# Kernel optimization log

Hardware: AMD Instinct MI355X
Metric: run time of the kernel (lower is better)

The kernel has to match this reference:

```python
import jax, jax.numpy as jnp
import numpy as np

NEG = -1e9  # finite stand-in for -inf so grads stay NaN-free
BLANK = 0

def _lse3(a, b, c):
    m = jnp.maximum(jnp.maximum(a, b), c)
    return m + jnp.log(jnp.exp(a - m) + jnp.exp(b - m) + jnp.exp(c - m))

def setup_inputs() -> dict:
    key = jax.random.key(0)
    k1, k2, k3, k4 = jax.random.split(key, 4)
    T, B, C, S = 1024, 128, 256, 128
    logits = jax.random.normal(k1, (T, B, C), dtype=jnp.float32)
    log_probs = jax.nn.log_softmax(logits, axis=-1)  # CTCLoss expects log-probs
    y = jax.random.randint(k2, (B, S), 1, C)                 # labels in [1, C), never blank
    input_lengths = jax.random.randint(k3, (B,), 768, T + 1)  # 768..T
    target_lengths = jax.random.randint(k4, (B,), 64, S + 1)  # 64..S
    return {"log_probs": log_probs, "y": y,
            "input_lengths": input_lengths, "target_lengths": target_lengths}

def _ctc_loss(log_probs, y, input_lengths, target_lengths):
    T, B, C = log_probs.shape
    S = y.shape[1]
    L = 2 * S + 1  # extended label sequence: blank, y1, blank, y2, ..., blank

    ext = jnp.zeros((B, L), dtype=y.dtype).at[:, 1::2].set(y)  # even slots = blank(0)
    pos = jnp.arange(L)
    prev2 = jnp.concatenate([jnp.full((B, 2), BLANK, dtype=ext.dtype), ext[:, :-2]], axis=1)
    allow_skip = (pos[None, :] >= 2) & (ext != BLANK) & (ext != prev2)  # [B, L]

    # init alpha at t=0: only s=0 (blank) and s=1 (first label) reachable
    lp0 = log_probs[0]  # [B, C]
    alpha0 = jnp.full((B, L), NEG, dtype=log_probs.dtype)
    alpha0 = alpha0.at[:, 0].set(lp0[:, BLANK])
    alpha0 = alpha0.at[:, 1].set(jnp.take_along_axis(lp0, ext[:, 1:2], axis=1)[:, 0])

    def step(alpha, xs):
        lp_t, t = xs  # lp_t: [B, C]
        a0 = alpha
        a1 = jnp.concatenate([jnp.full((B, 1), NEG, alpha.dtype), alpha[:, :-1]], axis=1)
        a2 = jnp.concatenate([jnp.full((B, 2), NEG, alpha.dtype), alpha[:, :-2]], axis=1)
        a2 = jnp.where(allow_skip, a2, NEG)
        emit = jnp.take_along_axis(lp_t, ext, axis=1)  # [B, L]
        new = _lse3(a0, a1, a2) + emit
        # freeze alpha for samples whose input has already ended
        new = jnp.where(t < input_lengths[:, None], new, alpha)
        return new, None

    ts = jnp.arange(1, T)
    alpha_T, _ = jax.lax.scan(step, alpha0, (log_probs[1:], ts))

    # final log-likelihood: logsumexp of alpha at positions 2*tl and 2*tl-1
    idx_hi = (2 * target_lengths)[:, None]       # [B,1]
    idx_lo = (2 * target_lengths - 1)[:, None]
    a_hi = jnp.take_along_axis(alpha_T, idx_hi, axis=1)[:, 0]
    a_lo = jnp.take_along_axis(alpha_T, idx_lo, axis=1)[:, 0]
    m = jnp.maximum(a_hi, a_lo)
    ll = m + jnp.log(jnp.exp(a_hi - m) + jnp.exp(a_lo - m))
    loss = -ll  # per-sample negative log-likelihood

    # zero_infinity=True: zero out infeasible (effectively -inf likelihood) samples
    loss = jnp.where(loss < 0.5 * (-NEG), loss, 0.0)

    # reduction='mean': divide each loss by its target length, then batch mean
    return jnp.mean(loss / target_lengths.astype(loss.dtype))

def reference(log_probs, y, input_lengths, target_lengths):
    return _ctc_loss(log_probs, y, input_lengths, target_lengths)
```

## Files before the change

kernel.cpp:

```cpp
#include <hip/hip_runtime.h>


#define PF 8
#define CTC_C 256

__device__ __forceinline__ void renorm(double& Oa, double& Ob, double& Ea,
                                       double& Eb, double& E128, double& logC) {
  double m = fmax(fmax(Oa, Ob), fmax(Ea, Eb));
#pragma unroll
  for (int off = 32; off > 0; off >>= 1)
    m = fmax(m, __shfl_xor(m, off));
  m = fmax(m, E128);
  if (m > 0.) {
    long long bits = __double_as_longlong(m);
    int eb = (int)((bits >> 52) & 0x7ff);
    int e = eb - 1022;
    double s = __longlong_as_double((long long)(2045 - eb) << 52);
    Oa *= s; Ob *= s; Ea *= s; Eb *= s; E128 *= s;
    logC += (double)e * 0.6931471805599453;
  }
}

__global__ __launch_bounds__(64)
void ctc_fwd(const float* __restrict__ lp, const int* __restrict__ y,
             const int* __restrict__ ilen, const int* __restrict__ tlen,
             float* __restrict__ out, int T, int B, int S) {
  const int b = blockIdx.x;
  const int l = threadIdx.x;
  const long rowstride = (long)B * CTC_C;

  const int len = ilen[b];
  const int tl  = tlen[b];

  const int ya = y[(size_t)b * S + 2 * l];
  const int yb = y[(size_t)b * S + 2 * l + 1];
  const int yprev = __shfl_up(yb, 1);
  const bool skipA = (l > 0) && (ya != yprev);
  const bool skipB = (yb != ya);

  const float* row0 = lp + (size_t)b * CTC_C;
  const int y0 = y[(size_t)b * S];
  double Ea = (l == 0) ? (double)__expf(row0[0])  : 0.;
  double Oa = (l == 0) ? (double)__expf(row0[y0]) : 0.;
  double Eb = 0., Ob = 0., E128 = 0.;
  double logC = 0.;

  float pA[PF], pB[PF], pQ[PF];
#pragma unroll
  for (int d = 0; d < PF; ++d) {
    int t = 1 + d; t = (t < T) ? t : (T - 1);
    const float* r = lp + (size_t)t * rowstride + (size_t)b * CTC_C;
    pA[d] = r[ya]; pB[d] = r[yb]; pQ[d] = r[0];
  }

  const int nsteps = len - 1;
  const int nchunks = nsteps / PF;
  int t0 = 1;

  for (int c = 0; c < nchunks; ++c) {
#pragma unroll
    for (int d = 0; d < PF; ++d) {
      const int t = t0 + d;
      double pa = (double)__expf(pA[d]);
      double pb = (double)__expf(pB[d]);
      double pq = (double)__expf(pQ[d]);
      int tn = t + PF; tn = (tn < T) ? tn : (T - 1);
      const float* r = lp + (size_t)tn * rowstride + (size_t)b * CTC_C;
      pA[d] = r[ya]; pB[d] = r[yb]; pQ[d] = r[0];

      double Opm1 = __shfl_up(Ob, 1);
      Opm1 = (l == 0) ? 0. : Opm1;
      double O127 = __shfl(Ob, 63);

      double nOa = (Oa + Ea + (skipA ? Opm1 : 0.)) * pa;
      double nOb = (Ob + Eb + (skipB ? Oa   : 0.)) * pb;
      double nEa = (Ea + Opm1) * pq;
      double nEb = (Eb + Oa) * pq;
      E128 = (E128 + O127) * pq;
      Oa = nOa; Ob = nOb; Ea = nEa; Eb = nEb;

      if ((d & 7) == 7) renorm(Oa, Ob, Ea, Eb, E128, logC);
    }
    t0 += PF;
  }

#pragma unroll
  for (int d = 0; d < PF; ++d) {
    const int t = t0 + d;
    if (t <= nsteps) {
      double pa = (double)__expf(pA[d]);
      double pb = (double)__expf(pB[d]);
      double pq = (double)__expf(pQ[d]);
      double Opm1 = __shfl_up(Ob, 1);
      Opm1 = (l == 0) ? 0. : Opm1;
      double O127 = __shfl(Ob, 63);
      double nOa = (Oa + Ea + (skipA ? Opm1 : 0.)) * pa;
      double nOb = (Ob + Eb + (skipB ? Oa   : 0.)) * pb;
      double nEa = (Ea + Opm1) * pq;
      double nEb = (Eb + Oa) * pq;
      E128 = (E128 + O127) * pq;
      Oa = nOa; Ob = nOb; Ea = nEa; Eb = nEb;
      if ((d & 7) == 7) renorm(Oa, Ob, Ea, Eb, E128, logC);
    }
  }

  double vEa = __shfl(Ea, (tl >> 1) & 63);
  double vEb = __shfl(Eb, (tl >> 1) & 63);
  double vhi = (tl == S) ? E128 : ((tl & 1) ? vEb : vEa);
  int s2 = tl - 1;
  double vOa = __shfl(Oa, (s2 >> 1) & 63);
  double vOb = __shfl(Ob, (s2 >> 1) & 63);
  double vlo = (s2 & 1) ? vOb : vOa;

  double sum = vhi + vlo;
  double loss;
  if (sum > 0.) {
    loss = -(logC + log(sum));
  } else {
    loss = 1e30;
  }
  if (!(loss < 5.0e8)) loss = 0.;
  float contrib = (float)(loss / (double)tl / (double)B);
  if (l == 0) atomicAdd(out, contrib);
}

extern "C" void kernel_launch(void* const* d_in, const int* in_sizes, int n_in,
                              void* d_out, int out_size, void* d_ws, size_t ws_size,
                              hipStream_t stream) {
  const float* lp   = (const float*)d_in[0];
  const int*   yy   = (const int*)d_in[1];
  const int*   ilen = (const int*)d_in[2];
  const int*   tlen = (const int*)d_in[3];
  float* out = (float*)d_out;

  int B = in_sizes[2];
  int S = in_sizes[1] / B;
  int T = in_sizes[0] / (B * CTC_C);

  hipMemsetAsync(out, 0, sizeof(float), stream);
  ctc_fwd<<<B, 64, 0, stream>>>(lp, yy, ilen, tlen, out, T, B, S);
}
```

Before: 297.3 us.

## Restructure CTC recurrence: biased exp2, branchless masks, single shuffle, sparser renorm

Replaces expf with exp2f on a fused multiply-add that adds a constant exponent bias (2^9) per step, and subtracts the bias analytically at the end. The per-step shuffle of Ob is reorganized so only one shuffle (of the new Ob) is needed and the per-lane E128 update no longer needs a broadcast. Skip conditions become multiplicative masks feeding fma, prefetch pointers are advanced incrementally, and renormalization runs every 16 steps instead of 8. This targets the serial per-timestep latency chain of the wave, at some risk of overflow or underflow margin since renorm is less frequent.

```diff
diff --git a/kernel.cpp b/kernel.cpp
--- a/kernel.cpp
+++ b/kernel.cpp
@@ -3,23 +3,9 @@
 
 #define PF 8
 #define CTC_C 256
-
-__device__ __forceinline__ void renorm(double& Oa, double& Ob, double& Ea,
-                                       double& Eb, double& E128, double& logC) {
-  double m = fmax(fmax(Oa, Ob), fmax(Ea, Eb));
-#pragma unroll
-  for (int off = 32; off > 0; off >>= 1)
-    m = fmax(m, __shfl_xor(m, off));
-  m = fmax(m, E128);
-  if (m > 0.) {
-    long long bits = __double_as_longlong(m);
-    int eb = (int)((bits >> 52) & 0x7ff);
-    int e = eb - 1022;
-    double s = __longlong_as_double((long long)(2045 - eb) << 52);
-    Oa *= s; Ob *= s; Ea *= s; Eb *= s; E128 *= s;
-    logC += (double)e * 0.6931471805599453;
-  }
-}
+#define EXP_BIAS 9.0f
+#define LOG2E 1.4426950408889634f
+#define LN2 0.6931471805599453
 
 __global__ __launch_bounds__(64)
 void ctc_fwd(const float* __restrict__ lp, const int* __restrict__ y,
@@ -27,7 +13,7 @@
              float* __restrict__ out, int T, int B, int S) {
   const int b = blockIdx.x;
   const int l = threadIdx.x;
-  const long rowstride = (long)B * CTC_C;
+  const size_t rowstride = (size_t)B * CTC_C;
 
   const int len = ilen[b];
   const int tl  = tlen[b];
@@ -35,51 +21,71 @@
   const int ya = y[(size_t)b * S + 2 * l];
   const int yb = y[(size_t)b * S + 2 * l + 1];
   const int yprev = __shfl_up(yb, 1);
-  const bool skipA = (l > 0) && (ya != yprev);
-  const bool skipB = (yb != ya);
+  const double maskA = (ya != yprev) ? 1.0 : 0.0;
+  const double maskB = (yb != ya) ? 1.0 : 0.0;
 
   const float* row0 = lp + (size_t)b * CTC_C;
   const int y0 = y[(size_t)b * S];
-  double Ea = (l == 0) ? (double)__expf(row0[0])  : 0.;
-  double Oa = (l == 0) ? (double)__expf(row0[y0]) : 0.;
-  double Eb = 0., Ob = 0., E128 = 0.;
-  double logC = 0.;
+  double Ea = (l == 0) ? (double)__expf(row0[0])  : 0.0;
+  double Oa = (l == 0) ? (double)__expf(row0[y0]) : 0.0;
+  double Eb = 0.0, Ob = 0.0, E128 = 0.0;
+  double Opm1 = 0.0;
+  int e_sum = 0;
 
   float pA[PF], pB[PF], pQ[PF];
+  {
+    const float* r = lp + rowstride + (size_t)b * CTC_C;
+    const float* rl = lp + (size_t)(T - 1) * rowstride + (size_t)b * CTC_C;
 #pragma unroll
-  for (int d = 0; d < PF; ++d) {
-    int t = 1 + d; t = (t < T) ? t : (T - 1);
-    const float* r = lp + (size_t)t * rowstride + (size_t)b * CTC_C;
-    pA[d] = r[ya]; pB[d] = r[yb]; pQ[d] = r[0];
+    for (int d = 0; d < PF; ++d) {
+      const float* rp = (1 + d <= T - 1) ? r : rl;
+      pA[d] = rp[ya]; pB[d] = rp[yb]; pQ[d] = rp[0];
+      r += rowstride;
+    }
   }
 
   const int nsteps = len - 1;
   const int nchunks = nsteps / PF;
+  const float* rlast = lp + (size_t)(T - 1) * rowstride + (size_t)b * CTC_C;
+  const float* rfill = lp + (size_t)(1 + PF) * rowstride + (size_t)b * CTC_C;
   int t0 = 1;
 
   for (int c = 0; c < nchunks; ++c) {
 #pragma unroll
     for (int d = 0; d < PF; ++d) {
       const int t = t0 + d;
-      double pa = (double)__expf(pA[d]);
-      double pb = (double)__expf(pB[d]);
-      double pq = (double)__expf(pQ[d]);
-      int tn = t + PF; tn = (tn < T) ? tn : (T - 1);
-      const float* r = lp + (size_t)tn * rowstride + (size_t)b * CTC_C;
-      pA[d] = r[ya]; pB[d] = r[yb]; pQ[d] = r[0];
+      const float* rp = (t + PF <= T - 1) ? rfill : rlast;
+      float nA = rp[ya], nB = rp[yb], nQ = rp[0];
+      rfill += rowstride;
 
-      double Opm1 = __shfl_up(Ob, 1);
-      Opm1 = (l == 0) ? 0. : Opm1;
-      double O127 = __shfl(Ob, 63);
+      float fa = exp2f(fmaf(pA[d], LOG2E, EXP_BIAS));
+      float fb = exp2f(fmaf(pB[d], LOG2E, EXP_BIAS));
+      float fq = exp2f(fmaf(pQ[d], LOG2E, EXP_BIAS));
+      pA[d] = nA; pB[d] = nB; pQ[d] = nQ;
+      double pa = (double)fa, pb = (double)fb, pq = (double)fq;
 
-      double nOa = (Oa + Ea + (skipA ? Opm1 : 0.)) * pa;
-      double nOb = (Ob + Eb + (skipB ? Oa   : 0.)) * pb;
+      double nOb = fma(maskB, Oa, Ob + Eb) * pb;
+      double up = __shfl_up(nOb, 1);
+      double nOa = fma(maskA, Opm1, Oa + Ea) * pa;
       double nEa = (Ea + Opm1) * pq;
       double nEb = (Eb + Oa) * pq;
-      E128 = (E128 + O127) * pq;
+      E128 = (E128 + Ob) * pq;
       Oa = nOa; Ob = nOb; Ea = nEa; Eb = nEb;
+      Opm1 = (l == 0) ? 0.0 : up;
 
-      if ((d & 7) == 7) renorm(Oa, Ob, Ea, Eb, E128, logC);
+      if (d == PF - 1 && (c & 1)) {
+        double m = fmax(fmax(Oa, Ob), fmax(Ea, Eb));
+        m = fmax(m, E128);
+#pragma unroll
+        for (int off = 32; off > 0; off >>= 1)
+          m = fmax(m, __shfl_xor(m, off));
+        long long bits = __double_as_longlong(m);
+        int eb2 = (int)((bits >> 52) & 0x7ff);
+        int e = eb2 - 1022;
+        double s = __longlong_as_double((long long)(2045 - eb2) << 52);
+        Oa *= s; Ob *= s; Ea *= s; Eb *= s; E128 *= s; Opm1 *= s;
+        e_sum += e;
+      }
     }
     t0 += PF;
   }
@@ -88,38 +94,39 @@
   for (int d = 0; d < PF; ++d) {
     const int t = t0 + d;
     if (t <= nsteps) {
-      double pa = (double)__expf(pA[d]);
-      double pb = (double)__expf(pB[d]);
-      double pq = (double)__expf(pQ[d]);
-      double Opm1 = __shfl_up(Ob, 1);
-      Opm1 = (l == 0) ? 0. : Opm1;
-      double O127 = __shfl(Ob, 63);
-      double nOa = (Oa + Ea + (skipA ? Opm1 : 0.)) * pa;
-      double nOb = (Ob + Eb + (skipB ? Oa   : 0.)) * pb;
+      float fa = exp2f(fmaf(pA[d], LOG2E, EXP_BIAS));
+      float fb = exp2f(fmaf(pB[d], LOG2E, EXP_BIAS));
+      float fq = exp2f(fmaf(pQ[d], LOG2E, EXP_BIAS));
+      double pa = (double)fa, pb = (double)fb, pq = (double)fq;
+      double nOb = fma(maskB, Oa, Ob + Eb) * pb;
+      double up = __shfl_up(nOb, 1);
+      double nOa = fma(maskA, Opm1, Oa + Ea) * pa;
       double nEa = (Ea + Opm1) * pq;
       double nEb = (Eb + Oa) * pq;
-      E128 = (E128 + O127) * pq;
+      E128 = (E128 + Ob) * pq;
       Oa = nOa; Ob = nOb; Ea = nEa; Eb = nEb;
-      if ((d & 7) == 7) renorm(Oa, Ob, Ea, Eb, E128, logC);
+      Opm1 = (l == 0) ? 0.0 : up;
     }
   }
 
+  E128 = __shfl(E128, 63);
   double vEa = __shfl(Ea, (tl >> 1) & 63);
   double vEb = __shfl(Eb, (tl >> 1) & 63);
   double vhi = (tl == S) ? E128 : ((tl & 1) ? vEb : vEa);
-  int s2 = tl - 1;
+  const int s2 = tl - 1;
   double vOa = __shfl(Oa, (s2 >> 1) & 63);
   double vOb = __shfl(Ob, (s2 >> 1) & 63);
   double vlo = (s2 & 1) ? vOb : vOa;
 
   double sum = vhi + vlo;
   double loss;
-  if (sum > 0.) {
-    loss = -(logC + log(sum));
+  if (sum > 0.0) {
+    double ll = log(sum) + (double)(e_sum - 9 * nsteps) * LN2;
+    loss = -ll;
   } else {
     loss = 1e30;
   }
-  if (!(loss < 5.0e8)) loss = 0.;
+  if (!(loss < 5.0e8)) loss = 0.0;
   float contrib = (float)(loss / (double)tl / (double)B);
   if (l == 0) atomicAdd(out, contrib);
 }
```

New measurement: 307.2 us. 1.03x slower.
